# Kernel tuning notes

Measured on AMD Instinct MI355X. Metric: run time of the kernel, lower is better.

The kernel has to match this reference:

```python
import jax, jax.numpy as jnp
import numpy as np
from jax import lax

C = 173            # EEG channels (independent towers)
L = 400            # samples per channel
POOL_OUT = 10      # AdaptiveMaxPool1d output length (400/10 = 40 exact window)
EPS = 1e-5


def setup_inputs() -> dict:
    key = jax.random.key(0)
    ks = jax.random.split(key, 6)
    B = 64
    x = jax.random.normal(ks[0], (B, C, L), dtype=jnp.float32)
    # per-channel tower 1: Conv1d(1,16,9)  -> grouped kernel [C*16, 1, 9]
    w1 = jax.random.normal(ks[1], (C * 16, 1, 9), dtype=jnp.float32) * 0.2
    b1 = jnp.zeros((C * 16,), jnp.float32)
    g1 = jnp.ones((C * 16,), jnp.float32)
    beta1 = jnp.zeros((C * 16,), jnp.float32)
    m1 = jnp.zeros((C * 16,), jnp.float32)
    v1 = jnp.ones((C * 16,), jnp.float32)
    # per-channel tower 2: Conv1d(16,32,7) -> grouped kernel [C*32, 16, 7]
    w2 = jax.random.normal(ks[2], (C * 32, 16, 7), dtype=jnp.float32) * 0.05
    b2 = jnp.zeros((C * 32,), jnp.float32)
    g2 = jnp.ones((C * 32,), jnp.float32)
    beta2 = jnp.zeros((C * 32,), jnp.float32)
    m2 = jnp.zeros((C * 32,), jnp.float32)
    v2 = jnp.ones((C * 32,), jnp.float32)
    # combiner MLP: Linear(32*C*10, 128) -> ReLU -> Linear(128, 1)
    wc1 = jax.random.normal(ks[3], (128, 32 * C * POOL_OUT), dtype=jnp.float32) * 0.01
    bc1 = jnp.zeros((128,), jnp.float32)
    wc2 = jax.random.normal(ks[4], (1, 128), dtype=jnp.float32) * 0.05
    bc2 = jnp.zeros((1,), jnp.float32)
    return dict(x=x, w1=w1, b1=b1, g1=g1, beta1=beta1, m1=m1, v1=v1,
                w2=w2, b2=b2, g2=g2, beta2=beta2, m2=m2, v2=v2,
                wc1=wc1, bc1=bc1, wc2=wc2, bc2=bc2)


def _bn(y, g, beta, m, v):
    # inference-mode BatchNorm1d over channel axis of [B, CF, L]
    inv = g * lax.rsqrt(v + EPS)
    return y * inv[None, :, None] + (beta - m * inv)[None, :, None]


def reference(x, w1, b1, g1, beta1, m1, v1, w2, b2, g2, beta2, m2, v2, wc1, bc1, wc2, bc2):
    B = x.shape[0]
    dn = ('NCH', 'OIH', 'NCH')
    # tower conv 1: all 173 per-channel Conv1d(1,16,9,pad=4) as one grouped conv
    y = lax.conv_general_dilated(x, w1, (1,), [(4, 4)], dimension_numbers=dn,
                                 feature_group_count=C)           # [B, C*16, 400]
    y = jax.nn.relu(_bn(y + b1[None, :, None], g1, beta1, m1, v1))
    # tower conv 2: Conv1d(16,32,7,pad=3), grouped by channel
    y = lax.conv_general_dilated(y, w2, (1,), [(3, 3)], dimension_numbers=dn,
                                 feature_group_count=C)           # [B, C*32, 400]
    y = jax.nn.relu(_bn(y + b2[None, :, None], g2, beta2, m2, v2))
    # AdaptiveMaxPool1d(10): exact non-overlapping windows of 40
    y = y.reshape(B, C * 32, POOL_OUT, L // POOL_OUT).max(axis=-1)  # [B, C*32, 10]
    # concat of per-channel flattened features == flatten (channel, feat, pos)
    flat = y.reshape(B, C * 32 * POOL_OUT)                          # [B, 55360]
    h = jax.nn.relu(flat @ wc1.T + bc1)
    out = h @ wc2.T + bc2                                           # [B, 1]
    return out
```

## Files before the change

### kernel.cpp

```cpp
#include <hip/hip_runtime.h>

#define C_CH 173
#define L_IN 400
#define EPSV 1e-5f
#define KFEAT 55360

typedef __fp16   fp16x2 __attribute__((ext_vector_type(2)));
typedef _Float16 f16x8  __attribute__((ext_vector_type(8)));
typedef float    f32x4  __attribute__((ext_vector_type(4)));
typedef float    f32x16 __attribute__((ext_vector_type(16)));

#define Y1T_STRIDE_I 9
#define Y1T_ROWS   406

#define SEG_STRIDE 102

#define N1 (173 * 3584)
#define N2 (173 * 512)
#define N3 (173 * 96)
#define NH 8192

__global__ __launch_bounds__(256) void prep_kernel(
    const float* __restrict__ w1, const float* __restrict__ b1,
    const float* __restrict__ g1, const float* __restrict__ beta1,
    const float* __restrict__ m1, const float* __restrict__ v1,
    const float* __restrict__ w2, const float* __restrict__ b2,
    const float* __restrict__ g2, const float* __restrict__ beta2,
    const float* __restrict__ m2, const float* __restrict__ v2,
    _Float16* __restrict__ w2T_g, _Float16* __restrict__ w1T_g,
    float* __restrict__ sc_g, float* __restrict__ h_ws)
{
    const int idx = blockIdx.x * 256 + threadIdx.x;
    if (idx < N1) {
        int c = idx / 3584, r = idx - c * 3584;
        int dt = r >> 9, fg = r & 511;
        int f = fg >> 4, g = fg & 15;
        w2T_g[idx] = (_Float16)w2[c * 3584 + f * 112 + g * 7 + dt];
    } else if (idx < N1 + N2) {
        int j = idx - N1;
        int c = j / 512, r = j - c * 512;
        int g = r >> 5, k = r & 31;
        w1T_g[j] = (k < 9) ? (_Float16)w1[c * 144 + g * 9 + k] : (_Float16)0.0f;
    } else if (idx < N1 + N2 + N3) {
        int j = idx - N1 - N2;
        int c = j / 96, r = j - c * 96;
        float o;
        if (r < 32) {
            int g  = r & 15;
            int cf = c * 16 + g;
            float inv = g1[cf] * rsqrtf(v1[cf] + EPSV);
            o = (r < 16) ? inv : (b1[cf] - m1[cf]) * inv + beta1[cf];
        } else {
            int f  = (r - 32) & 31;
            int cf = c * 32 + f;
            float inv = g2[cf] * rsqrtf(v2[cf] + EPSV);
            o = (r < 64) ? inv : (b2[cf] - m2[cf]) * inv + beta2[cf];
        }
        sc_g[j] = o;
    } else if (idx < N1 + N2 + N3 + NH) {
        h_ws[idx - N1 - N2 - N3] = 0.0f;
    }
}

__global__ __launch_bounds__(320, 7) void tower_kernel(
    const float* __restrict__ x,
    const _Float16* __restrict__ w2T_g, const _Float16* __restrict__ w1T_g,
    const float* __restrict__ sc_g,
    _Float16* __restrict__ featH)
{
    __shared__ __align__(16) _Float16 xa_s[432];
    __shared__ __align__(16) _Float16 xb_s[432];
    __shared__ __align__(16) _Float16 w1T_s[16 * 32];
    __shared__ __align__(16) _Float16 y1T_s[Y1T_ROWS * 2 * Y1T_STRIDE_I];
    __shared__ __align__(16) _Float16 w2T_s[7 * 512];
    __shared__ _Float16               segmax_s[32 * SEG_STRIDE];
    __shared__ __align__(16) float    cst_s[96];

    const int c   = blockIdx.x;
    const int tid = threadIdx.x;

    {
        const int4* w2src = (const int4*)(w2T_g + (size_t)c * 3584);
        for (int i = tid; i < 448; i += 320) ((int4*)w2T_s)[i] = w2src[i];
        const int4* w1src = (const int4*)(w1T_g + c * 512);
        if (tid < 64) ((int4*)w1T_s)[tid] = w1src[tid];
        const float4* csrc = (const float4*)(sc_g + c * 96);
        if (tid >= 64 && tid < 88) ((float4*)cst_s)[tid - 64] = csrc[tid - 64];
        if (tid >= 88 && tid < 142) {
            int i = tid - 88;
            int r = i / 9, cx = i - r * 9;
            int row = (r < 3) ? r : (400 + r);
            ((int*)y1T_s)[row * Y1T_STRIDE_I + cx] = 0;
        }
    }
    __syncthreads();
    const float s2f  = cst_s[32 + (tid & 31)];
    const float sh2f = cst_s[64 + (tid & 31)];

    const int nlaneH = tid & 31;
    const int halfH  = (tid >> 5) & 1;
    union F8q { int4 q; f16x8 h; } af[7];
#pragma unroll
    for (int dt = 0; dt < 7; ++dt)
        af[dt].q = *(const int4*)((const int*)w2T_s + dt * 256 + nlaneH * 8 + halfH * 4);

    for (int nb = 0; nb < 4; ++nb) {
        const int b = blockIdx.y * 4 + nb;

        const float* xrow = x + ((size_t)b * C_CH + c) * L_IN;
        for (int i = tid; i < 432; i += 320) {
            float v = (i >= 4 && i < 404) ? xrow[i - 4] : 0.0f;
            _Float16 h = (_Float16)v;
            xa_s[i] = h;
            if (i > 0) xb_s[i - 1] = h;
        }
        if (tid == 0) xb_s[431] = (_Float16)0.0f;
        __syncthreads();

        {
            const int lane = tid & 63;
            const int wv5  = tid >> 6;
            const int nl   = lane & 15;
            const int q    = lane >> 4;
            union { int4 v; f16x8 h; } a1;
            a1.v = *(const int4*)((const int*)w1T_s + nl * 16 + q * 4);
            float s1r[4], sh1r[4];
#pragma unroll
            for (int r = 0; r < 4; ++r) {
                s1r[r]  = cst_s[q * 4 + r];
                sh1r[r] = cst_s[16 + q * 4 + r];
            }
            const int* xsel = (const int*)((nl & 1) ? xb_s : xa_s);
            for (int tile = 0; tile < 5; ++tile) {
                const int t0 = (wv5 * 5 + tile) * 16;
                const int dw = (t0 + nl + q * 8) >> 1;
                union { int4 v; f16x8 h; } bf;
                bf.v.x = xsel[dw];
                bf.v.y = xsel[dw + 1];
                bf.v.z = xsel[dw + 2];
                bf.v.w = xsel[dw + 3];
                f32x4 acc = {0.0f, 0.0f, 0.0f, 0.0f};
                acc = __builtin_amdgcn_mfma_f32_16x16x32_f16(a1.h, bf.h, acc, 0, 0, 0);
                union { _Float16 h[4]; int2 d; } pk;
#pragma unroll
                for (int r = 0; r < 4; ++r) {
                    float v = acc[r] * s1r[r] + sh1r[r];
                    pk.h[r] = (_Float16)(v > 0.0f ? v : 0.0f);
                }
                int* yp = (int*)y1T_s + (t0 + nl + 3) * Y1T_STRIDE_I + q * 2;
                yp[0] = pk.d.x;
                yp[1] = pk.d.y;
            }
        }
        __syncthreads();

        {
            const int wv    = tid >> 6;
            const int nlane = nlaneH;
            const int half  = halfH;

            for (int tile = wv; tile < 13; tile += 5) {
                const int tA  = tile * 32 + nlane;
                const int tAr = tA < 400 ? tA : 399;
                f32x16 acc;
#pragma unroll
                for (int i = 0; i < 16; ++i) acc[i] = 0.0f;

#pragma unroll
                for (int dt = 0; dt < 7; ++dt) {
                    const int* p = (const int*)y1T_s + (tAr + dt) * Y1T_STRIDE_I + half * 4;
                    union { int d[4]; f16x8 h; } bf;
                    bf.d[0] = p[0];
                    bf.d[1] = p[1];
                    bf.d[2] = p[2];
                    bf.d[3] = p[3];
                    acc = __builtin_amdgcn_mfma_f32_32x32x16_f16(bf.h, af[dt].h, acc, 0, 0, 0);
                }

                const int base = nlane * SEG_STRIDE + tile * 8 + half;
#pragma unroll
                for (int q = 0; q < 4; ++q) {
                    float v0 = acc[4 * q + 0] * s2f;
                    float v1 = acc[4 * q + 1] * s2f;
                    float v2 = acc[4 * q + 2] * s2f;
                    float v3 = acc[4 * q + 3] * s2f;
                    float m  = fmaxf(fmaxf(v0, v1), fmaxf(v2, v3));
                    const int sub = tile * 8 + 2 * q + half;
                    if (sub < 100) segmax_s[base + 2 * q] = (_Float16)m;
                }
            }
        }
        __syncthreads();

        {
            const int f = tid & 31;
            const int p = tid >> 5;
            float m = -3.0e38f;
#pragma unroll
            for (int k = 0; k < 10; ++k)
                m = fmaxf(m, (float)segmax_s[f * SEG_STRIDE + p * 10 + k]);
            float v = fmaxf(m + sh2f, 0.0f);
            featH[(size_t)b * KFEAT + (c * 32 + f) * 10 + p] = (_Float16)v;
        }
    }
}

__global__ __launch_bounds__(512) void fc1_kernel(
    const _Float16* __restrict__ featH, const float* __restrict__ wc1,
    float* __restrict__ h_ws)
{
    __shared__ float red[4 * 1024];

    const int tid   = threadIdx.x;
    const int w     = tid >> 6;
    const int lane  = tid & 63;
    const int nlane = lane & 31;
    const int half  = lane >> 5;
    const int kh    = w >> 2;
    const int jq    = w & 3;
    const int jrow  = jq * 32 + nlane;
    const int bh    = blockIdx.y;
    const int k0    = blockIdx.x * 320 + kh * 160;

    const float*    ap  = wc1   + (size_t)jrow * KFEAT + k0 + half * 8;
    const _Float16* b0p = featH + (size_t)(bh * 32 + nlane) * KFEAT + k0 + half * 8;

    f32x16 acc0;
#pragma unroll
    for (int i = 0; i < 16; ++i) acc0[i] = 0.0f;

#pragma unroll 5
    for (int s = 0; s < 10; ++s) {
        const float4 aw0 = *(const float4*)(ap + s * 16);
        const float4 aw1 = *(const float4*)(ap + s * 16 + 4);
        union { fp16x2 v2[4]; f16x8 h; } a;
        a.v2[0] = __builtin_amdgcn_cvt_pkrtz(aw0.x, aw0.y);
        a.v2[1] = __builtin_amdgcn_cvt_pkrtz(aw0.z, aw0.w);
        a.v2[2] = __builtin_amdgcn_cvt_pkrtz(aw1.x, aw1.y);
        a.v2[3] = __builtin_amdgcn_cvt_pkrtz(aw1.z, aw1.w);

        union { int4 q; f16x8 h; } b0;
        b0.q = *(const int4*)(b0p + s * 16);

        acc0 = __builtin_amdgcn_mfma_f32_32x32x16_f16(a.h, b0.h, acc0, 0, 0, 0);
    }

    if (kh == 1) {
        float* rp = red + jq * 1024;
#pragma unroll
        for (int reg = 0; reg < 16; ++reg)
            rp[(reg * 2 + half) * 32 + nlane] = acc0[reg];
    }
    __syncthreads();
    if (kh == 0) {
        const float* rp = red + jq * 1024;
#pragma unroll
        for (int reg = 0; reg < 16; ++reg) {
            int j = jq * 32 + (reg & 3) + 8 * (reg >> 2) + 4 * half;
            float v0 = acc0[reg] + rp[(reg * 2 + half) * 32 + nlane];
            atomicAdd(&h_ws[j * 64 + bh * 32 + nlane], v0);
        }
    }
}

__global__ __launch_bounds__(512) void fc2_kernel(
    const float* __restrict__ h_ws, const float* __restrict__ bc1,
    const float* __restrict__ wc2, const float* __restrict__ bc2,
    float* __restrict__ out)
{
    __shared__ float partial[512];
    const int t  = threadIdx.x;
    const int b  = t & 63;
    const int jc = t >> 6;
    float s = 0.0f;
#pragma unroll
    for (int jj = 0; jj < 16; ++jj) {
        const int j = jc * 16 + jj;
        float hv = h_ws[j * 64 + b] + bc1[j];
        hv = hv > 0.0f ? hv : 0.0f;
        s += wc2[j] * hv;
    }
    partial[t] = s;
    __syncthreads();
    if (t < 64) {
        float r = partial[t];
#pragma unroll
        for (int k = 1; k < 8; ++k) r += partial[t + 64 * k];
        out[b] = r + bc2[0];
    }
}

extern "C" void kernel_launch(void* const* d_in, const int* in_sizes, int n_in,
                              void* d_out, int out_size, void* d_ws, size_t ws_size,
                              hipStream_t stream)
{
    const float* x     = (const float*)d_in[0];
    const float* w1    = (const float*)d_in[1];
    const float* b1    = (const float*)d_in[2];
    const float* g1    = (const float*)d_in[3];
    const float* beta1 = (const float*)d_in[4];
    const float* m1    = (const float*)d_in[5];
    const float* v1    = (const float*)d_in[6];
    const float* w2    = (const float*)d_in[7];
    const float* b2    = (const float*)d_in[8];
    const float* g2    = (const float*)d_in[9];
    const float* beta2 = (const float*)d_in[10];
    const float* m2    = (const float*)d_in[11];
    const float* v2    = (const float*)d_in[12];
    const float* wc1   = (const float*)d_in[13];
    const float* bc1   = (const float*)d_in[14];
    const float* wc2   = (const float*)d_in[15];
    const float* bc2   = (const float*)d_in[16];

    char* ws = (char*)d_ws;
    _Float16* featH = (_Float16*)ws;
    _Float16* w2T_g = (_Float16*)(ws + 7086080);
    _Float16* w1T_g = (_Float16*)(ws + 8326144);
    float*    sc_g  = (float*)(ws + 8503296);
    float*    h_ws  = (float*)(ws + 8569728);

    hipLaunchKernelGGL(prep_kernel, dim3(2865), dim3(256), 0, stream,
                       w1, b1, g1, beta1, m1, v1,
                       w2, b2, g2, beta2, m2, v2, w2T_g, w1T_g, sc_g, h_ws);

    hipLaunchKernelGGL(tower_kernel, dim3(C_CH, 16), dim3(320), 0, stream,
                       x, w2T_g, w1T_g, sc_g, featH);

    hipLaunchKernelGGL(fc1_kernel, dim3(173, 2), dim3(512), 0, stream,
                       featH, wc1, h_ws);

    hipLaunchKernelGGL(fc2_kernel, dim3(1), dim3(512), 0, stream,
                       h_ws, bc1, wc2, bc2, (float*)d_out);
}
```

Before: 190.9 us.

## Store fc1 operands in MFMA fragment layout and cover both batch halves per block

The tower kernel now writes pooled features directly in the per-lane MFMA B-fragment order, so fc1 loads them as contiguous int4 vectors. Each fc1 block now processes all 64 batch rows with two accumulators, so each wc1 weight tile is read and converted once instead of once per batch half. When the workspace is large enough, the prep kernel also converts wc1 to fp16 in A-fragment order every call, and fc1 reads that packed copy. The intent is to cut wc1 traffic and conversion work and make fc1 loads coalesced. The cost is extra prep work and memory traffic per call to write the fp16 weight copy, which runs serially before the tower kernel.

New measurement: 199.7 us. 1.05x slower.

```diff
diff --git a/kernel.cpp b/kernel.cpp
--- a/kernel.cpp
+++ b/kernel.cpp
@@ -19,6 +19,9 @@
 #define N2 (173 * 512)
 #define N3 (173 * 96)
 #define NH 8192
+#define NA4 885760
+#define PREP_BASE (N1 + N2 + N3 + NH)
+
 
 __global__ __launch_bounds__(256) void prep_kernel(
     const float* __restrict__ w1, const float* __restrict__ b1,
@@ -27,8 +30,10 @@
     const float* __restrict__ w2, const float* __restrict__ b2,
     const float* __restrict__ g2, const float* __restrict__ beta2,
     const float* __restrict__ m2, const float* __restrict__ v2,
+    const float* __restrict__ wc1,
     _Float16* __restrict__ w2T_g, _Float16* __restrict__ w1T_g,
-    float* __restrict__ sc_g, float* __restrict__ h_ws)
+    float* __restrict__ sc_g, float* __restrict__ h_ws,
+    _Float16* __restrict__ afrag_g, int doA)
 {
     const int idx = blockIdx.x * 256 + threadIdx.x;
     if (idx < N1) {
@@ -57,8 +62,28 @@
             o = (r < 64) ? inv : (b2[cf] - m2[cf]) * inv + beta2[cf];
         }
         sc_g[j] = o;
-    } else if (idx < N1 + N2 + N3 + NH) {
+    } else if (idx < PREP_BASE) {
         h_ws[idx - N1 - N2 - N3] = 0.0f;
+    } else if (doA) {
+        const int i = idx - PREP_BASE;
+        if (i >= NA4) return;
+        const int lane = i & 63;
+        int t = i >> 6;
+        const int jq = t & 3; t >>= 2;
+        const int s  = t % 10; t /= 10;
+        const int kh = t & 1;
+        const int c  = t >> 1;
+        const int j  = jq * 32 + (lane & 31);
+        const int kg = c * 320 + kh * 160 + s * 16 + (lane >> 5) * 8;
+        const float* wp = wc1 + (size_t)j * KFEAT + kg;
+        const float4 a0 = *(const float4*)wp;
+        const float4 a1 = *(const float4*)(wp + 4);
+        union { fp16x2 v2[4]; int4 q; } a;
+        a.v2[0] = __builtin_amdgcn_cvt_pkrtz(a0.x, a0.y);
+        a.v2[1] = __builtin_amdgcn_cvt_pkrtz(a0.z, a0.w);
+        a.v2[2] = __builtin_amdgcn_cvt_pkrtz(a1.x, a1.y);
+        a.v2[3] = __builtin_amdgcn_cvt_pkrtz(a1.z, a1.w);
+        ((int4*)afrag_g)[i] = a.q;
     }
 }
 
@@ -66,7 +91,7 @@
     const float* __restrict__ x,
     const _Float16* __restrict__ w2T_g, const _Float16* __restrict__ w1T_g,
     const float* __restrict__ sc_g,
-    _Float16* __restrict__ featH)
+    _Float16* __restrict__ featF)
 {
     __shared__ __align__(16) _Float16 xa_s[432];
     __shared__ __align__(16) _Float16 xb_s[432];
@@ -200,18 +225,82 @@
             for (int k = 0; k < 10; ++k)
                 m = fmaxf(m, (float)segmax_s[f * SEG_STRIDE + p * 10 + k]);
             float v = fmaxf(m + sh2f, 0.0f);
-            featH[(size_t)b * KFEAT + (c * 32 + f) * 10 + p] = (_Float16)v;
-        }
-    }
-}
-
-__global__ __launch_bounds__(512) void fc1_kernel(
-    const _Float16* __restrict__ featH, const float* __restrict__ wc1,
+            const int kl = f * 10 + p;
+            const int kh2 = (kl >= 160) ? 1 : 0;
+            const int kr  = kl - kh2 * 160;
+            const int s   = kr >> 4;
+            const int ko  = kr & 15;
+            const int addr = ((((c * 2 + kh2) * 10 + s) * 2 + (b >> 5)) * 64
+                              + (ko >> 3) * 32 + (b & 31)) * 8 + (ko & 7);
+            featF[addr] = (_Float16)v;
+        }
+    }
+}
+
+__global__ __launch_bounds__(512) void fc1_frag_kernel(
+    const _Float16* __restrict__ featF, const _Float16* __restrict__ afrag,
     float* __restrict__ h_ws)
 {
-    __shared__ float red[4 * 1024];
+    __shared__ float red[4 * 2048];
 
     const int tid   = threadIdx.x;
+    const int c     = blockIdx.x;
+    const int w     = tid >> 6;
+    const int lane  = tid & 63;
+    const int nlane = lane & 31;
+    const int half  = lane >> 5;
+    const int kh    = w >> 2;
+    const int jq    = w & 3;
+
+    const int4* Ap = (const int4*)afrag +
+                     ((size_t)(c * 2 + kh) * 40 + jq) * 64 + lane;
+    const int4* Bp = (const int4*)featF +
+                     (size_t)(c * 2 + kh) * 1280 + lane;
+
+    f32x16 acc0, acc1;
+#pragma unroll
+    for (int i = 0; i < 16; ++i) { acc0[i] = 0.0f; acc1[i] = 0.0f; }
+
+#pragma unroll
+    for (int s = 0; s < 10; ++s) {
+        union { int4 q; f16x8 h; } a, b0, b1;
+        a.q  = Ap[s * 256];
+        b0.q = Bp[s * 128];
+        b1.q = Bp[s * 128 + 64];
+        acc0 = __builtin_amdgcn_mfma_f32_32x32x16_f16(a.h, b0.h, acc0, 0, 0, 0);
+        acc1 = __builtin_amdgcn_mfma_f32_32x32x16_f16(a.h, b1.h, acc1, 0, 0, 0);
+    }
+
+    if (kh == 1) {
+        float* rp = red + jq * 2048;
+#pragma unroll
+        for (int reg = 0; reg < 16; ++reg) {
+            rp[(reg * 2 + half) * 64 + nlane]      = acc0[reg];
+            rp[(reg * 2 + half) * 64 + 32 + nlane] = acc1[reg];
+        }
+    }
+    __syncthreads();
+    if (kh == 0) {
+        const float* rp = red + jq * 2048;
+#pragma unroll
+        for (int reg = 0; reg < 16; ++reg) {
+            int j = jq * 32 + (reg & 3) + 8 * (reg >> 2) + 4 * half;
+            float v0 = acc0[reg] + rp[(reg * 2 + half) * 64 + nlane];
+            float v1 = acc1[reg] + rp[(reg * 2 + half) * 64 + 32 + nlane];
+            atomicAdd(&h_ws[j * 64 + nlane], v0);
+            atomicAdd(&h_ws[j * 64 + 32 + nlane], v1);
+        }
+    }
+}
+
+__global__ __launch_bounds__(512) void fc1_fb_kernel(
+    const _Float16* __restrict__ featF, const float* __restrict__ wc1,
+    float* __restrict__ h_ws)
+{
+    __shared__ float red[4 * 2048];
+
+    const int tid   = threadIdx.x;
+    const int c     = blockIdx.x;
     const int w     = tid >> 6;
     const int lane  = tid & 63;
     const int nlane = lane & 31;
@@ -219,15 +308,13 @@
     const int kh    = w >> 2;
     const int jq    = w & 3;
     const int jrow  = jq * 32 + nlane;
-    const int bh    = blockIdx.y;
-    const int k0    = blockIdx.x * 320 + kh * 160;
-
-    const float*    ap  = wc1   + (size_t)jrow * KFEAT + k0 + half * 8;
-    const _Float16* b0p = featH + (size_t)(bh * 32 + nlane) * KFEAT + k0 + half * 8;
-
-    f32x16 acc0;
-#pragma unroll
-    for (int i = 0; i < 16; ++i) acc0[i] = 0.0f;
+
+    const float* ap = wc1 + (size_t)jrow * KFEAT + c * 320 + kh * 160 + half * 8;
+    const int4*  Bp = (const int4*)featF + (size_t)(c * 2 + kh) * 1280 + lane;
+
+    f32x16 acc0, acc1;
+#pragma unroll
+    for (int i = 0; i < 16; ++i) { acc0[i] = 0.0f; acc1[i] = 0.0f; }
 
 #pragma unroll 5
     for (int s = 0; s < 10; ++s) {
@@ -239,26 +326,32 @@
         a.v2[2] = __builtin_amdgcn_cvt_pkrtz(aw1.x, aw1.y);
         a.v2[3] = __builtin_amdgcn_cvt_pkrtz(aw1.z, aw1.w);
 
-        union { int4 q; f16x8 h; } b0;
-        b0.q = *(const int4*)(b0p + s * 16);
+        union { int4 q; f16x8 h; } b0, b1;
+        b0.q = Bp[s * 128];
+        b1.q = Bp[s * 128 + 64];
 
         acc0 = __builtin_amdgcn_mfma_f32_32x32x16_f16(a.h, b0.h, acc0, 0, 0, 0);
+        acc1 = __builtin_amdgcn_mfma_f32_32x32x16_f16(a.h, b1.h, acc1, 0, 0, 0);
     }
 
     if (kh == 1) {
-        float* rp = red + jq * 1024;
-#pragma unroll
-        for (int reg = 0; reg < 16; ++reg)
-            rp[(reg * 2 + half) * 32 + nlane] = acc0[reg];
+        float* rp = red + jq * 2048;
+#pragma unroll
+        for (int reg = 0; reg < 16; ++reg) {
+            rp[(reg * 2 + half) * 64 + nlane]      = acc0[reg];
+            rp[(reg * 2 + half) * 64 + 32 + nlane] = acc1[reg];
+        }
     }
     __syncthreads();
     if (kh == 0) {
-        const float* rp = red + jq * 1024;
+        const float* rp = red + jq * 2048;
 #pragma unroll
         for (int reg = 0; reg < 16; ++reg) {
             int j = jq * 32 + (reg & 3) + 8 * (reg >> 2) + 4 * half;
-            float v0 = acc0[reg] + rp[(reg * 2 + half) * 32 + nlane];
-            atomicAdd(&h_ws[j * 64 + bh * 32 + nlane], v0);
+            float v0 = acc0[reg] + rp[(reg * 2 + half) * 64 + nlane];
+            float v1 = acc1[reg] + rp[(reg * 2 + half) * 64 + 32 + nlane];
+            atomicAdd(&h_ws[j * 64 + nlane], v0);
+            atomicAdd(&h_ws[j * 64 + 32 + nlane], v1);
         }
     }
 }
@@ -313,21 +406,30 @@
     const float* bc2   = (const float*)d_in[16];
 
     char* ws = (char*)d_ws;
-    _Float16* featH = (_Float16*)ws;
+    _Float16* featF = (_Float16*)ws;
     _Float16* w2T_g = (_Float16*)(ws + 7086080);
     _Float16* w1T_g = (_Float16*)(ws + 8326144);
     float*    sc_g  = (float*)(ws + 8503296);
     float*    h_ws  = (float*)(ws + 8569728);
-
-    hipLaunchKernelGGL(prep_kernel, dim3(2865), dim3(256), 0, stream,
+    _Float16* afrag = (_Float16*)(ws + 8602496);
+
+    const int useFrag = (ws_size >= (size_t)22774656) ? 1 : 0;
+
+    hipLaunchKernelGGL(prep_kernel, dim3(useFrag ? 6325 : 2865), dim3(256), 0, stream,
                        w1, b1, g1, beta1, m1, v1,
-                       w2, b2, g2, beta2, m2, v2, w2T_g, w1T_g, sc_g, h_ws);
+                       w2, b2, g2, beta2, m2, v2, wc1,
+                       w2T_g, w1T_g, sc_g, h_ws, afrag, useFrag);
 
     hipLaunchKernelGGL(tower_kernel, dim3(C_CH, 16), dim3(320), 0, stream,
-                       x, w2T_g, w1T_g, sc_g, featH);
-
-    hipLaunchKernelGGL(fc1_kernel, dim3(173, 2), dim3(512), 0, stream,
-                       featH, wc1, h_ws);
+                       x, w2T_g, w1T_g, sc_g, featF);
+
+    if (useFrag) {
+        hipLaunchKernelGGL(fc1_frag_kernel, dim3(173), dim3(512), 0, stream,
+                           featF, afrag, h_ws);
+    } else {
+        hipLaunchKernelGGL(fc1_fb_kernel, dim3(173), dim3(512), 0, stream,
+                           featF, wc1, h_ws);
+    }
 
     hipLaunchKernelGGL(fc2_kernel, dim3(1), dim3(512), 0, stream,
                        h_ws, bc1, wc2, bc2, (float*)d_out);
```

## Fold weight prep into tower kernel and fc2 into fc1 via last-block reduction

Applied to the files above, without the earlier changes.

Removes the separate prep kernel: each tower block now transposes and converts its own w2/w1 slices to fp16 and computes the BN constants in shared memory, and it zeros the h workspace and counter. fc1 now processes all 64 batch rows per block with two MFMA accumulators, halving the grid and reading each wc1 tile once instead of twice. fc2 is folded into fc1 through an atomic completion counter, so the last block computes the final output. This cuts two kernel launches and the global round trips for the prepared weights. In exchange, every tower block (16 per channel) repeats the strided weight conversion, and a grid-wide counter handshake is added.

Result: slower. 199.6 us (+4.6%).

```diff
diff --git a/kernel.cpp b/kernel.cpp
--- a/kernel.cpp
+++ b/kernel.cpp
@@ -15,58 +15,16 @@
 
 #define SEG_STRIDE 102
 
-#define N1 (173 * 3584)
-#define N2 (173 * 512)
-#define N3 (173 * 96)
-#define NH 8192
-
-__global__ __launch_bounds__(256) void prep_kernel(
+__global__ __launch_bounds__(320, 7) void tower_kernel(
+    const float* __restrict__ x,
     const float* __restrict__ w1, const float* __restrict__ b1,
     const float* __restrict__ g1, const float* __restrict__ beta1,
     const float* __restrict__ m1, const float* __restrict__ v1,
     const float* __restrict__ w2, const float* __restrict__ b2,
     const float* __restrict__ g2, const float* __restrict__ beta2,
     const float* __restrict__ m2, const float* __restrict__ v2,
-    _Float16* __restrict__ w2T_g, _Float16* __restrict__ w1T_g,
-    float* __restrict__ sc_g, float* __restrict__ h_ws)
-{
-    const int idx = blockIdx.x * 256 + threadIdx.x;
-    if (idx < N1) {
-        int c = idx / 3584, r = idx - c * 3584;
-        int dt = r >> 9, fg = r & 511;
-        int f = fg >> 4, g = fg & 15;
-        w2T_g[idx] = (_Float16)w2[c * 3584 + f * 112 + g * 7 + dt];
-    } else if (idx < N1 + N2) {
-        int j = idx - N1;
-        int c = j / 512, r = j - c * 512;
-        int g = r >> 5, k = r & 31;
-        w1T_g[j] = (k < 9) ? (_Float16)w1[c * 144 + g * 9 + k] : (_Float16)0.0f;
-    } else if (idx < N1 + N2 + N3) {
-        int j = idx - N1 - N2;
-        int c = j / 96, r = j - c * 96;
-        float o;
-        if (r < 32) {
-            int g  = r & 15;
-            int cf = c * 16 + g;
-            float inv = g1[cf] * rsqrtf(v1[cf] + EPSV);
-            o = (r < 16) ? inv : (b1[cf] - m1[cf]) * inv + beta1[cf];
-        } else {
-            int f  = (r - 32) & 31;
-            int cf = c * 32 + f;
-            float inv = g2[cf] * rsqrtf(v2[cf] + EPSV);
-            o = (r < 64) ? inv : (b2[cf] - m2[cf]) * inv + beta2[cf];
-        }
-        sc_g[j] = o;
-    } else if (idx < N1 + N2 + N3 + NH) {
-        h_ws[idx - N1 - N2 - N3] = 0.0f;
-    }
-}
-
-__global__ __launch_bounds__(320, 7) void tower_kernel(
-    const float* __restrict__ x,
-    const _Float16* __restrict__ w2T_g, const _Float16* __restrict__ w1T_g,
-    const float* __restrict__ sc_g,
-    _Float16* __restrict__ featH)
+    _Float16* __restrict__ featH, float* __restrict__ h_ws,
+    unsigned int* __restrict__ cnt)
 {
     __shared__ __align__(16) _Float16 xa_s[432];
     __shared__ __align__(16) _Float16 xb_s[432];
@@ -80,17 +38,40 @@
     const int tid = threadIdx.x;
 
     {
-        const int4* w2src = (const int4*)(w2T_g + (size_t)c * 3584);
-        for (int i = tid; i < 448; i += 320) ((int4*)w2T_s)[i] = w2src[i];
-        const int4* w1src = (const int4*)(w1T_g + c * 512);
-        if (tid < 64) ((int4*)w1T_s)[tid] = w1src[tid];
-        const float4* csrc = (const float4*)(sc_g + c * 96);
-        if (tid >= 64 && tid < 88) ((float4*)cst_s)[tid - 64] = csrc[tid - 64];
-        if (tid >= 88 && tid < 142) {
-            int i = tid - 88;
+        const float* w2c = w2 + (size_t)c * 3584;
+        for (int i = tid; i < 3584; i += 320) {
+            int dt = i >> 9, fg = i & 511;
+            int f = fg >> 4, g = fg & 15;
+            w2T_s[i] = (_Float16)w2c[f * 112 + g * 7 + dt];
+        }
+        const float* w1c = w1 + c * 144;
+        for (int i = tid; i < 512; i += 320) {
+            int g = i >> 5, k = i & 31;
+            w1T_s[i] = (k < 9) ? (_Float16)w1c[g * 9 + k] : (_Float16)0.0f;
+        }
+        if (tid < 96) {
+            int r = tid;
+            float o;
+            if (r < 32) {
+                int cf = c * 16 + (r & 15);
+                float inv = g1[cf] * rsqrtf(v1[cf] + EPSV);
+                o = (r < 16) ? inv : (b1[cf] - m1[cf]) * inv + beta1[cf];
+            } else {
+                int cf = c * 32 + ((r - 32) & 31);
+                float inv = g2[cf] * rsqrtf(v2[cf] + EPSV);
+                o = (r < 64) ? inv : (b2[cf] - m2[cf]) * inv + beta2[cf];
+            }
+            cst_s[r] = o;
+        }
+        if (tid >= 96 && tid < 150) {
+            int i = tid - 96;
             int r = i / 9, cx = i - r * 9;
             int row = (r < 3) ? r : (400 + r);
             ((int*)y1T_s)[row * Y1T_STRIDE_I + cx] = 0;
+        }
+        if (blockIdx.y == 0) {
+            if (c < 32 && tid < 256) h_ws[c * 256 + tid] = 0.0f;
+            if (c == 32 && tid == 0)  cnt[0] = 0u;
         }
     }
     __syncthreads();
@@ -207,9 +188,13 @@
 
 __global__ __launch_bounds__(512) void fc1_kernel(
     const _Float16* __restrict__ featH, const float* __restrict__ wc1,
-    float* __restrict__ h_ws)
+    const float* __restrict__ bc1, const float* __restrict__ wc2,
+    const float* __restrict__ bc2,
+    float* __restrict__ h_ws, unsigned int* __restrict__ cnt,
+    float* __restrict__ out)
 {
-    __shared__ float red[4 * 1024];
+    __shared__ float red[4 * 2048];
+    __shared__ unsigned int isLast;
 
     const int tid   = threadIdx.x;
     const int w     = tid >> 6;
@@ -219,15 +204,15 @@
     const int kh    = w >> 2;
     const int jq    = w & 3;
     const int jrow  = jq * 32 + nlane;
-    const int bh    = blockIdx.y;
     const int k0    = blockIdx.x * 320 + kh * 160;
 
     const float*    ap  = wc1   + (size_t)jrow * KFEAT + k0 + half * 8;
-    const _Float16* b0p = featH + (size_t)(bh * 32 + nlane) * KFEAT + k0 + half * 8;
-
-    f32x16 acc0;
-#pragma unroll
-    for (int i = 0; i < 16; ++i) acc0[i] = 0.0f;
+    const _Float16* b0p = featH + (size_t)nlane * KFEAT + k0 + half * 8;
+    const _Float16* b1p = featH + (size_t)(nlane + 32) * KFEAT + k0 + half * 8;
+
+    f32x16 acc0, acc1;
+#pragma unroll
+    for (int i = 0; i < 16; ++i) { acc0[i] = 0.0f; acc1[i] = 0.0f; }
 
 #pragma unroll 5
     for (int s = 0; s < 10; ++s) {
@@ -239,54 +224,65 @@
         a.v2[2] = __builtin_amdgcn_cvt_pkrtz(aw1.x, aw1.y);
         a.v2[3] = __builtin_amdgcn_cvt_pkrtz(aw1.z, aw1.w);
 
-        union { int4 q; f16x8 h; } b0;
+        union { int4 q; f16x8 h; } b0, b1;
         b0.q = *(const int4*)(b0p + s * 16);
+        b1.q = *(const int4*)(b1p + s * 16);
 
         acc0 = __builtin_amdgcn_mfma_f32_32x32x16_f16(a.h, b0.h, acc0, 0, 0, 0);
+        acc1 = __builtin_amdgcn_mfma_f32_32x32x16_f16(a.h, b1.h, acc1, 0, 0, 0);
     }
 
     if (kh == 1) {
-        float* rp = red + jq * 1024;
-#pragma unroll
-        for (int reg = 0; reg < 16; ++reg)
-            rp[(reg * 2 + half) * 32 + nlane] = acc0[reg];
+        float* rp = red + jq * 2048;
+#pragma unroll
+        for (int reg = 0; reg < 16; ++reg) {
+            rp[(reg * 2 + half) * 64 + nlane]      = acc0[reg];
+            rp[(reg * 2 + half) * 64 + 32 + nlane] = acc1[reg];
+        }
     }
     __syncthreads();
     if (kh == 0) {
-        const float* rp = red + jq * 1024;
+        const float* rp = red + jq * 2048;
 #pragma unroll
         for (int reg = 0; reg < 16; ++reg) {
             int j = jq * 32 + (reg & 3) + 8 * (reg >> 2) + 4 * half;
-            float v0 = acc0[reg] + rp[(reg * 2 + half) * 32 + nlane];
-            atomicAdd(&h_ws[j * 64 + bh * 32 + nlane], v0);
-        }
-    }
-}
-
-__global__ __launch_bounds__(512) void fc2_kernel(
-    const float* __restrict__ h_ws, const float* __restrict__ bc1,
-    const float* __restrict__ wc2, const float* __restrict__ bc2,
-    float* __restrict__ out)
-{
-    __shared__ float partial[512];
-    const int t  = threadIdx.x;
-    const int b  = t & 63;
-    const int jc = t >> 6;
-    float s = 0.0f;
-#pragma unroll
-    for (int jj = 0; jj < 16; ++jj) {
-        const int j = jc * 16 + jj;
-        float hv = h_ws[j * 64 + b] + bc1[j];
-        hv = hv > 0.0f ? hv : 0.0f;
-        s += wc2[j] * hv;
-    }
-    partial[t] = s;
+            float v0 = acc0[reg] + rp[(reg * 2 + half) * 64 + nlane];
+            float v1 = acc1[reg] + rp[(reg * 2 + half) * 64 + 32 + nlane];
+            atomicAdd(&h_ws[j * 64 + nlane], v0);
+            atomicAdd(&h_ws[j * 64 + 32 + nlane], v1);
+        }
+    }
+
     __syncthreads();
-    if (t < 64) {
-        float r = partial[t];
-#pragma unroll
-        for (int k = 1; k < 8; ++k) r += partial[t + 64 * k];
-        out[b] = r + bc2[0];
+    if (tid == 0) {
+        __threadfence();
+        unsigned int old = __hip_atomic_fetch_add(
+            cnt, 1u, __ATOMIC_ACQ_REL, __HIP_MEMORY_SCOPE_AGENT);
+        isLast = (old == (unsigned int)(C_CH - 1)) ? 1u : 0u;
+    }
+    __syncthreads();
+    if (isLast) {
+        __threadfence();
+        const int b  = tid & 63;
+        const int jc = tid >> 6;
+        float s = 0.0f;
+#pragma unroll
+        for (int jj = 0; jj < 16; ++jj) {
+            const int j = jc * 16 + jj;
+            float hv = __hip_atomic_load(&h_ws[j * 64 + b],
+                                         __ATOMIC_RELAXED,
+                                         __HIP_MEMORY_SCOPE_AGENT) + bc1[j];
+            hv = hv > 0.0f ? hv : 0.0f;
+            s += wc2[j] * hv;
+        }
+        red[tid] = s;
+        __syncthreads();
+        if (tid < 64) {
+            float r = red[tid];
+#pragma unroll
+            for (int k = 1; k < 8; ++k) r += red[tid + 64 * k];
+            out[tid] = r + bc2[0];
+        }
     }
 }
 
@@ -313,22 +309,15 @@
     const float* bc2   = (const float*)d_in[16];
 
     char* ws = (char*)d_ws;
-    _Float16* featH = (_Float16*)ws;
-    _Float16* w2T_g = (_Float16*)(ws + 7086080);
-    _Float16* w1T_g = (_Float16*)(ws + 8326144);
-    float*    sc_g  = (float*)(ws + 8503296);
-    float*    h_ws  = (float*)(ws + 8569728);
-
-    hipLaunchKernelGGL(prep_kernel, dim3(2865), dim3(256), 0, stream,
-                       w1, b1, g1, beta1, m1, v1,
-                       w2, b2, g2, beta2, m2, v2, w2T_g, w1T_g, sc_g, h_ws);
+    _Float16*     featH = (_Float16*)ws;
+    float*        h_ws  = (float*)(ws + 7086080);
+    unsigned int* cnt   = (unsigned int*)(ws + 7118848);
 
     hipLaunchKernelGGL(tower_kernel, dim3(C_CH, 16), dim3(320), 0, stream,
-                       x, w2T_g, w1T_g, sc_g, featH);
-
-    hipLaunchKernelGGL(fc1_kernel, dim3(173, 2), dim3(512), 0, stream,
-                       featH, wc1, h_ws);
-
-    hipLaunchKernelGGL(fc2_kernel, dim3(1), dim3(512), 0, stream,
-                       h_ws, bc1, wc2, bc2, (float*)d_out);
+                       x, w1, b1, g1, beta1, m1, v1,
+                       w2, b2, g2, beta2, m2, v2,
+                       featH, h_ws, cnt);
+
+    hipLaunchKernelGGL(fc1_kernel, dim3(C_CH), dim3(512), 0, stream,
+                       featH, wc1, bc1, wc2, bc2, h_ws, cnt, (float*)d_out);
 }
```

## Cover full batch per fc1 block and replace atomics with partial-sum reduction

Applied to the files above, without the earlier changes.

Each fc1 block now handles all 64 batch rows with two MFMA accumulators, so every wc1 element is loaded and converted once instead of twice. Instead of atomically adding into a zeroed h buffer, blocks write per-k-block partial sums that a new reduce kernel sums deterministically. This drops the zeroing from prep and the atomic contention. In exchange there is an extra kernel launch, about 5.6 MB of partial-sum traffic, half as many fc1 blocks, and higher register and LDS use per block.

Measured after the change: 196.8 us. +3.1%, slower.

```diff
diff --git a/kernel.cpp b/kernel.cpp
--- a/kernel.cpp
+++ b/kernel.cpp
@@ -18,7 +18,6 @@
 #define N1 (173 * 3584)
 #define N2 (173 * 512)
 #define N3 (173 * 96)
-#define NH 8192
 
 __global__ __launch_bounds__(256) void prep_kernel(
     const float* __restrict__ w1, const float* __restrict__ b1,
@@ -28,7 +27,7 @@
     const float* __restrict__ g2, const float* __restrict__ beta2,
     const float* __restrict__ m2, const float* __restrict__ v2,
     _Float16* __restrict__ w2T_g, _Float16* __restrict__ w1T_g,
-    float* __restrict__ sc_g, float* __restrict__ h_ws)
+    float* __restrict__ sc_g)
 {
     const int idx = blockIdx.x * 256 + threadIdx.x;
     if (idx < N1) {
@@ -57,8 +56,6 @@
             o = (r < 64) ? inv : (b2[cf] - m2[cf]) * inv + beta2[cf];
         }
         sc_g[j] = o;
-    } else if (idx < N1 + N2 + N3 + NH) {
-        h_ws[idx - N1 - N2 - N3] = 0.0f;
     }
 }
 
@@ -207,11 +204,12 @@
 
 __global__ __launch_bounds__(512) void fc1_kernel(
     const _Float16* __restrict__ featH, const float* __restrict__ wc1,
-    float* __restrict__ h_ws)
-{
-    __shared__ float red[4 * 1024];
+    float* __restrict__ part)
+{
+    __shared__ float red[4 * 2048];
 
     const int tid   = threadIdx.x;
+    const int kb    = blockIdx.x;
     const int w     = tid >> 6;
     const int lane  = tid & 63;
     const int nlane = lane & 31;
@@ -219,15 +217,15 @@
     const int kh    = w >> 2;
     const int jq    = w & 3;
     const int jrow  = jq * 32 + nlane;
-    const int bh    = blockIdx.y;
-    const int k0    = blockIdx.x * 320 + kh * 160;
+    const int k0    = kb * 320 + kh * 160;
 
     const float*    ap  = wc1   + (size_t)jrow * KFEAT + k0 + half * 8;
-    const _Float16* b0p = featH + (size_t)(bh * 32 + nlane) * KFEAT + k0 + half * 8;
-
-    f32x16 acc0;
-#pragma unroll
-    for (int i = 0; i < 16; ++i) acc0[i] = 0.0f;
+    const _Float16* b0p = featH + (size_t)nlane * KFEAT + k0 + half * 8;
+    const _Float16* b1p = featH + (size_t)(nlane + 32) * KFEAT + k0 + half * 8;
+
+    f32x16 acc0, acc1;
+#pragma unroll
+    for (int i = 0; i < 16; ++i) { acc0[i] = 0.0f; acc1[i] = 0.0f; }
 
 #pragma unroll 5
     for (int s = 0; s < 10; ++s) {
@@ -239,28 +237,52 @@
         a.v2[2] = __builtin_amdgcn_cvt_pkrtz(aw1.x, aw1.y);
         a.v2[3] = __builtin_amdgcn_cvt_pkrtz(aw1.z, aw1.w);
 
-        union { int4 q; f16x8 h; } b0;
+        union { int4 q; f16x8 h; } b0, b1;
         b0.q = *(const int4*)(b0p + s * 16);
+        b1.q = *(const int4*)(b1p + s * 16);
 
         acc0 = __builtin_amdgcn_mfma_f32_32x32x16_f16(a.h, b0.h, acc0, 0, 0, 0);
+        acc1 = __builtin_amdgcn_mfma_f32_32x32x16_f16(a.h, b1.h, acc1, 0, 0, 0);
     }
 
     if (kh == 1) {
-        float* rp = red + jq * 1024;
-#pragma unroll
-        for (int reg = 0; reg < 16; ++reg)
-            rp[(reg * 2 + half) * 32 + nlane] = acc0[reg];
+        float* rp = red + jq * 2048;
+#pragma unroll
+        for (int reg = 0; reg < 16; ++reg) {
+            rp[(reg * 2 + half) * 64 + nlane]      = acc0[reg];
+            rp[(reg * 2 + half) * 64 + 32 + nlane] = acc1[reg];
+        }
     }
     __syncthreads();
     if (kh == 0) {
-        const float* rp = red + jq * 1024;
+        const float* rp = red + jq * 2048;
+        float* pt = part + (size_t)kb * 8192;
 #pragma unroll
         for (int reg = 0; reg < 16; ++reg) {
             int j = jq * 32 + (reg & 3) + 8 * (reg >> 2) + 4 * half;
-            float v0 = acc0[reg] + rp[(reg * 2 + half) * 32 + nlane];
-            atomicAdd(&h_ws[j * 64 + bh * 32 + nlane], v0);
-        }
-    }
+            float v0 = acc0[reg] + rp[(reg * 2 + half) * 64 + nlane];
+            float v1 = acc1[reg] + rp[(reg * 2 + half) * 64 + 32 + nlane];
+            pt[j * 64 + nlane]      = v0;
+            pt[j * 64 + 32 + nlane] = v1;
+        }
+    }
+}
+
+__global__ __launch_bounds__(256) void reduce_kernel(
+    const float* __restrict__ part, float* __restrict__ h_ws)
+{
+    const int e = blockIdx.x * 256 + threadIdx.x;
+    const float* p = part + e;
+    float s0 = 0.0f, s1 = 0.0f, s2 = 0.0f, s3 = 0.0f;
+#pragma unroll 4
+    for (int kb = 0; kb < 172; kb += 4) {
+        s0 += p[(size_t)(kb + 0) * 8192];
+        s1 += p[(size_t)(kb + 1) * 8192];
+        s2 += p[(size_t)(kb + 2) * 8192];
+        s3 += p[(size_t)(kb + 3) * 8192];
+    }
+    s0 += p[(size_t)172 * 8192];
+    h_ws[e] = (s0 + s1) + (s2 + s3);
 }
 
 __global__ __launch_bounds__(512) void fc2_kernel(
@@ -314,20 +336,24 @@
 
     char* ws = (char*)d_ws;
     _Float16* featH = (_Float16*)ws;
-    _Float16* w2T_g = (_Float16*)(ws + 7086080);
-    _Float16* w1T_g = (_Float16*)(ws + 8326144);
-    float*    sc_g  = (float*)(ws + 8503296);
-    float*    h_ws  = (float*)(ws + 8569728);
-
-    hipLaunchKernelGGL(prep_kernel, dim3(2865), dim3(256), 0, stream,
+    float*    part  = (float*)(ws + 7086080);
+    _Float16* w2T_g = (_Float16*)(ws + 12754944);
+    _Float16* w1T_g = (_Float16*)(ws + 13995008);
+    float*    sc_g  = (float*)(ws + 14172160);
+    float*    h_ws  = (float*)(ws + 14238592);
+
+    hipLaunchKernelGGL(prep_kernel, dim3(2834), dim3(256), 0, stream,
                        w1, b1, g1, beta1, m1, v1,
-                       w2, b2, g2, beta2, m2, v2, w2T_g, w1T_g, sc_g, h_ws);
+                       w2, b2, g2, beta2, m2, v2, w2T_g, w1T_g, sc_g);
 
     hipLaunchKernelGGL(tower_kernel, dim3(C_CH, 16), dim3(320), 0, stream,
                        x, w2T_g, w1T_g, sc_g, featH);
 
-    hipLaunchKernelGGL(fc1_kernel, dim3(173, 2), dim3(512), 0, stream,
-                       featH, wc1, h_ws);
+    hipLaunchKernelGGL(fc1_kernel, dim3(C_CH), dim3(512), 0, stream,
+                       featH, wc1, part);
+
+    hipLaunchKernelGGL(reduce_kernel, dim3(32), dim3(256), 0, stream,
+                       part, h_ws);
 
     hipLaunchKernelGGL(fc2_kernel, dim3(1), dim3(512), 0, stream,
                        h_ws, bc1, wc2, bc2, (float*)d_out);
```
